# Optimization experiments

Hardware: AMD Instinct MI355X
Metric: run time of the kernel (lower is better)

## Reference

```python
import jax, jax.numpy as jnp
import numpy as np

PENALTY_FACTOR = 2.0
THRESHOLD = 0.01


def setup_inputs() -> dict:
    key = jax.random.key(0)
    k1, k2 = jax.random.split(key)
    B, N = 256, 65536
    prediction = jax.random.normal(k1, (B, N), dtype=jnp.float32)
    label = jax.random.normal(k2, (B, N), dtype=jnp.float32)
    return {"prediction": prediction, "label": label}


def _first_last_significant(mask, half):
    # mask: [B, half] bool. Returns per-row first/last True index,
    # defaulting to (0, half-1) when the row has no True entries
    # (matching the torch fallback branch).
    any_m = jnp.any(mask, axis=1)
    first = jnp.argmax(mask, axis=1)                      # 0 if all False
    last = (half - 1) - jnp.argmax(mask[:, ::-1], axis=1)  # half-1 if all False
    first = jnp.where(any_m, first, 0)
    last = jnp.where(any_m, last, half - 1)
    return first, last


def reference(prediction, label):
    B, N = label.shape
    half = N // 2
    label_real, label_imag = label[:, :half], label[:, half:]
    pred_real, pred_imag = prediction[:, :half], prediction[:, half:]

    label_phase = jnp.arctan2(label_imag, label_real)
    pred_phase = jnp.arctan2(pred_imag, pred_real)
    label_int = label_real ** 2 + label_imag ** 2
    pred_int = pred_real ** 2 + pred_imag ** 2

    fr, lr = _first_last_significant(jnp.abs(label_real) > THRESHOLD, half)
    fi, li = _first_last_significant(jnp.abs(label_imag) > THRESHOLD, half)

    idx = jnp.arange(half)[None, :]  # [1, half]
    w_real = jnp.where((idx < fr[:, None]) | (idx > lr[:, None]), PENALTY_FACTOR, 1.0)
    w_imag = jnp.where((idx < fi[:, None]) | (idx > li[:, None]), PENALTY_FACTOR, 1.0)

    mse_real = w_real * (pred_real - label_real) ** 2
    mse_imag = w_imag * (pred_imag - label_imag) ** 2
    mse_int = (pred_int - label_int) ** 2
    mse_phase = (pred_phase - label_phase) ** 2

    per_sample = (mse_real.mean(axis=1) + mse_imag.mean(axis=1)
                  + 50.0 * mse_int.mean(axis=1) + 0.0 * mse_phase.mean(axis=1))
    return per_sample.mean()
```

## Files before the change

### kernel.cpp

```cpp
#include <hip/hip_runtime.h>
#include <climits>

constexpr int HALF  = 32768;
constexpr int TPB   = 256;
constexpr int CHUNK = 2048;
constexpr int NCHNK = HALF / CHUNK;
constexpr float THRESH = 0.01f;

__global__ __launch_bounds__(TPB)
void main_kernel(const float* __restrict__ pred, const float* __restrict__ label,
                 float* __restrict__ part_sum, int4* __restrict__ part_idx)
{
    const int chunk = blockIdx.x, row = blockIdx.y;
    const int t = threadIdx.x, wave = t >> 6, lane = t & 63;

    const size_t rb4 = (size_t)row * (size_t)(2 * HALF / 4);
    const float4* lr4 = (const float4*)label + rb4;
    const float4* pr4 = (const float4*)pred + rb4;

    const int v0 = chunk * (CHUNK / 4) + t;
    const int v1 = v0 + TPB;
    const int H4 = HALF / 4;

    float4 a0 = lr4[v0],      a1 = lr4[v1];
    float4 b0 = lr4[v0 + H4], b1 = lr4[v1 + H4];
    float4 p0 = pr4[v0],      p1 = pr4[v1];
    float4 q0 = pr4[v0 + H4], q1 = pr4[v1 + H4];

    float sum = 0.f;
    int minr = INT_MAX, maxr = -1, mini = INT_MAX, maxi = -1;

#define STEP(ax, bx, px, qx, idx)                                 \
    {                                                             \
        float dr = (px) - (ax), di = (qx) - (bx);                 \
        float lint = (ax) * (ax) + (bx) * (bx);                   \
        float pint = (px) * (px) + (qx) * (qx);                   \
        float dd = pint - lint;                                   \
        sum += dr * dr + di * di + 50.f * dd * dd;                \
        if (fabsf(ax) > THRESH) {                                 \
            minr = min(minr, (idx)); maxr = max(maxr, (idx));     \
        }                                                         \
        if (fabsf(bx) > THRESH) {                                 \
            mini = min(mini, (idx)); maxi = max(maxi, (idx));     \
        }                                                         \
    }
    {
        const int base = v0 * 4;
        STEP(a0.x, b0.x, p0.x, q0.x, base + 0)
        STEP(a0.y, b0.y, p0.y, q0.y, base + 1)
        STEP(a0.z, b0.z, p0.z, q0.z, base + 2)
        STEP(a0.w, b0.w, p0.w, q0.w, base + 3)
    }
    {
        const int base = v1 * 4;
        STEP(a1.x, b1.x, p1.x, q1.x, base + 0)
        STEP(a1.y, b1.y, p1.y, q1.y, base + 1)
        STEP(a1.z, b1.z, p1.z, q1.z, base + 2)
        STEP(a1.w, b1.w, p1.w, q1.w, base + 3)
    }
#undef STEP

    #pragma unroll
    for (int off = 32; off > 0; off >>= 1) {
        sum += __shfl_down(sum, off);
        minr = min(minr, __shfl_down(minr, off));
        maxr = max(maxr, __shfl_down(maxr, off));
        mini = min(mini, __shfl_down(mini, off));
        maxi = max(maxi, __shfl_down(maxi, off));
    }

    __shared__ float s_sum[4];
    __shared__ int   s_idx[4][4];
    if (lane == 0) {
        s_sum[wave] = sum;
        s_idx[wave][0] = minr; s_idx[wave][1] = maxr;
        s_idx[wave][2] = mini; s_idx[wave][3] = maxi;
    }
    __syncthreads();
    if (t == 0) {
        float S = 0.f; int mr = INT_MAX, Mr = -1, mi = INT_MAX, Mi = -1;
        #pragma unroll
        for (int w = 0; w < 4; ++w) {
            S += s_sum[w];
            mr = min(mr, s_idx[w][0]); Mr = max(Mr, s_idx[w][1]);
            mi = min(mi, s_idx[w][2]); Mi = max(Mi, s_idx[w][3]);
        }
        const int slot = row * NCHNK + chunk;
        part_sum[slot] = S;
        part_idx[slot] = make_int4(mr, Mr, mi, Mi);
    }
}

__global__ __launch_bounds__(TPB)
void edge_kernel(const float* __restrict__ pred, const float* __restrict__ label,
                 const float* __restrict__ part_sum, const int4* __restrict__ part_idx,
                 float* __restrict__ row_tot)
{
    const int row = blockIdx.x;
    const int t = threadIdx.x, wave = t >> 6, lane = t & 63;

    float base = 0.f;
    int fr = INT_MAX, lastr = -1, fi = INT_MAX, lasti = -1;
    #pragma unroll
    for (int s = 0; s < NCHNK; ++s) {
        base += part_sum[row * NCHNK + s];
        int4 v = part_idx[row * NCHNK + s];
        fr = min(fr, v.x); lastr = max(lastr, v.y);
        fi = min(fi, v.z); lasti = max(lasti, v.w);
    }
    if (lastr < 0) { fr = 0; lastr = HALF - 1; }
    if (lasti < 0) { fi = 0; lasti = HALF - 1; }

    const float* Lr = label + (size_t)row * (2 * HALF);
    const float* Li = Lr + HALF;
    const float* Pr = pred + (size_t)row * (2 * HALF);
    const float* Pi = Pr + HALF;

    float ex = 0.f;
    for (int i = t; i < fr; i += TPB)               { float d = Pr[i] - Lr[i]; ex += d * d; }
    for (int i = lastr + 1 + t; i < HALF; i += TPB) { float d = Pr[i] - Lr[i]; ex += d * d; }
    for (int i = t; i < fi; i += TPB)               { float d = Pi[i] - Li[i]; ex += d * d; }
    for (int i = lasti + 1 + t; i < HALF; i += TPB) { float d = Pi[i] - Li[i]; ex += d * d; }

    #pragma unroll
    for (int off = 32; off > 0; off >>= 1) ex += __shfl_down(ex, off);
    __shared__ float s_ex[4];
    if (lane == 0) s_ex[wave] = ex;
    __syncthreads();
    if (t == 0)
        row_tot[row] = base + s_ex[0] + s_ex[1] + s_ex[2] + s_ex[3];
}

__global__ void finalize_kernel(const float* __restrict__ row_tot,
                                float* __restrict__ out, int rows)
{
    const int t = threadIdx.x;
    float v = 0.f;
    for (int i = t; i < rows; i += 256) v += row_tot[i];
    #pragma unroll
    for (int off = 32; off > 0; off >>= 1) v += __shfl_down(v, off);
    __shared__ float s[4];
    if ((t & 63) == 0) s[t >> 6] = v;
    __syncthreads();
    if (t == 0)
        out[0] = (s[0] + s[1] + s[2] + s[3]) * (1.0f / ((float)HALF * (float)rows));
}

extern "C" void kernel_launch(void* const* d_in, const int* in_sizes, int n_in,
                              void* d_out, int out_size, void* d_ws, size_t ws_size,
                              hipStream_t stream) {
    const float* pred  = (const float*)d_in[0];
    const float* label = (const float*)d_in[1];
    float* out = (float*)d_out;

    const int rows = in_sizes[0] / (2 * HALF);
    const int nslots = rows * NCHNK;

    float* part_sum = (float*)d_ws;
    int4*  part_idx = (int4*)((char*)d_ws + nslots * 4);
    float* row_tot  = (float*)((char*)d_ws + nslots * 4 + nslots * 16);

    dim3 gridA(NCHNK, rows);
    main_kernel<<<gridA, TPB, 0, stream>>>(pred, label, part_sum, part_idx);
    edge_kernel<<<rows, TPB, 0, stream>>>(pred, label, part_sum, part_idx, row_tot);
    finalize_kernel<<<1, 256, 0, stream>>>(row_tot, out, rows);
}
```

Measured before the change: 29.29 us.

## Fuse main, edge and finalize kernels into one cooperative kernel with grid syncs

Combines the three launches into a single cooperative kernel that uses grid-wide synchronization between the chunk reduction, per-row edge correction and final reduction phases. Intermediate partials are written and read with agent-scope atomic stores and loads. It is meant to remove inter-kernel launch gaps. The cooperative path is only used if occupancy allows all 4096 blocks to be co-resident, otherwise it falls back to the original three launches. Host-side occupancy queries are added on every call.

```diff
diff --git a/kernel.cpp b/kernel.cpp
--- a/kernel.cpp
+++ b/kernel.cpp
@@ -1,19 +1,36 @@
 #include <hip/hip_runtime.h>
+#include <hip/hip_cooperative_groups.h>
 #include <climits>
+
+namespace cg = cooperative_groups;
 
 constexpr int HALF  = 32768;
 constexpr int TPB   = 256;
 constexpr int CHUNK = 2048;
 constexpr int NCHNK = HALF / CHUNK;
+constexpr int ROWS  = 256;
+constexpr int NBLK  = NCHNK * ROWS;
 constexpr float THRESH = 0.01f;
 
-__global__ __launch_bounds__(TPB)
-void main_kernel(const float* __restrict__ pred, const float* __restrict__ label,
-                 float* __restrict__ part_sum, int4* __restrict__ part_idx)
-{
-    const int chunk = blockIdx.x, row = blockIdx.y;
-    const int t = threadIdx.x, wave = t >> 6, lane = t & 63;
-
+__device__ __forceinline__ void st_ag(float* p, float v) {
+    __hip_atomic_store(p, v, __ATOMIC_RELAXED, __HIP_MEMORY_SCOPE_AGENT);
+}
+__device__ __forceinline__ float ld_ag(const float* p) {
+    return __hip_atomic_load(p, __ATOMIC_RELAXED, __HIP_MEMORY_SCOPE_AGENT);
+}
+__device__ __forceinline__ void st_ag_i(int* p, int v) {
+    __hip_atomic_store(p, v, __ATOMIC_RELAXED, __HIP_MEMORY_SCOPE_AGENT);
+}
+__device__ __forceinline__ int ld_ag_i(const int* p) {
+    return __hip_atomic_load(p, __ATOMIC_RELAXED, __HIP_MEMORY_SCOPE_AGENT);
+}
+
+template <typename SUMF, typename IDXF>
+__device__ __forceinline__ void phase1_body(const float* __restrict__ pred,
+                                            const float* __restrict__ label,
+                                            int chunk, int row, int t, int wave, int lane,
+                                            SUMF&& emit_sum, IDXF&& emit_idx)
+{
     const size_t rb4 = (size_t)row * (size_t)(2 * HALF / 4);
     const float4* lr4 = (const float4*)label + rb4;
     const float4* pr4 = (const float4*)pred + rb4;
@@ -85,31 +102,136 @@
             mr = min(mr, s_idx[w][0]); Mr = max(Mr, s_idx[w][1]);
             mi = min(mi, s_idx[w][2]); Mi = max(Mi, s_idx[w][3]);
         }
+        emit_sum(S);
+        emit_idx(mr, Mr, mi, Mi);
+    }
+}
+
+__global__ __launch_bounds__(TPB, 8)
+void fused_kernel(const float* __restrict__ pred, const float* __restrict__ label,
+                  float* __restrict__ part_sum, int* __restrict__ part_idx,
+                  float* __restrict__ row_tot, float* __restrict__ out)
+{
+    cg::grid_group grid = cg::this_grid();
+    const int bid = blockIdx.x;
+    const int chunk = bid & (NCHNK - 1);
+    const int row = bid >> 4;
+    const int t = threadIdx.x, wave = t >> 6, lane = t & 63;
+
+    {
         const int slot = row * NCHNK + chunk;
-        part_sum[slot] = S;
-        part_idx[slot] = make_int4(mr, Mr, mi, Mi);
-    }
+        phase1_body(pred, label, chunk, row, t, wave, lane,
+            [&](float S) { st_ag(&part_sum[slot], S); },
+            [&](int mr, int Mr, int mi, int Mi) {
+                st_ag_i(&part_idx[slot * 4 + 0], mr);
+                st_ag_i(&part_idx[slot * 4 + 1], Mr);
+                st_ag_i(&part_idx[slot * 4 + 2], mi);
+                st_ag_i(&part_idx[slot * 4 + 3], Mi);
+            });
+    }
+
+    grid.sync();
+
+    if (bid < ROWS) {
+        const int r = bid;
+        __shared__ float sh_sum[NCHNK];
+        __shared__ int   sh_i[NCHNK][4];
+        if (t < NCHNK) {
+            const int slot = r * NCHNK + t;
+            sh_sum[t]  = ld_ag(&part_sum[slot]);
+            sh_i[t][0] = ld_ag_i(&part_idx[slot * 4 + 0]);
+            sh_i[t][1] = ld_ag_i(&part_idx[slot * 4 + 1]);
+            sh_i[t][2] = ld_ag_i(&part_idx[slot * 4 + 2]);
+            sh_i[t][3] = ld_ag_i(&part_idx[slot * 4 + 3]);
+        }
+        __syncthreads();
+
+        __shared__ float sh_base;
+        __shared__ int   sh_b[4];
+        if (t == 0) {
+            float S = 0.f; int fr = INT_MAX, lr = -1, fi = INT_MAX, li = -1;
+            #pragma unroll
+            for (int c = 0; c < NCHNK; ++c) {
+                S += sh_sum[c];
+                fr = min(fr, sh_i[c][0]); lr = max(lr, sh_i[c][1]);
+                fi = min(fi, sh_i[c][2]); li = max(li, sh_i[c][3]);
+            }
+            if (lr < 0) { fr = 0; lr = HALF - 1; }
+            if (li < 0) { fi = 0; li = HALF - 1; }
+            sh_base = S;
+            sh_b[0] = fr; sh_b[1] = lr; sh_b[2] = fi; sh_b[3] = li;
+        }
+        __syncthreads();
+        const int fr = sh_b[0], lr = sh_b[1], fi = sh_b[2], li = sh_b[3];
+
+        const float* Lr = label + (size_t)r * (2 * HALF);
+        const float* Li = Lr + HALF;
+        const float* Pr = pred + (size_t)r * (2 * HALF);
+        const float* Pi = Pr + HALF;
+
+        float ex = 0.f;
+        for (int i = t; i < fr; i += TPB)            { float d = Pr[i] - Lr[i]; ex += d * d; }
+        for (int i = lr + 1 + t; i < HALF; i += TPB) { float d = Pr[i] - Lr[i]; ex += d * d; }
+        for (int i = t; i < fi; i += TPB)            { float d = Pi[i] - Li[i]; ex += d * d; }
+        for (int i = li + 1 + t; i < HALF; i += TPB) { float d = Pi[i] - Li[i]; ex += d * d; }
+
+        #pragma unroll
+        for (int off = 32; off > 0; off >>= 1) ex += __shfl_down(ex, off);
+        __shared__ float s_ex[4];
+        if (lane == 0) s_ex[wave] = ex;
+        __syncthreads();
+        if (t == 0)
+            st_ag(&row_tot[r], sh_base + s_ex[0] + s_ex[1] + s_ex[2] + s_ex[3]);
+    }
+
+    grid.sync();
+
+    if (bid == 0) {
+        float v = (t < ROWS) ? ld_ag(&row_tot[t]) : 0.f;
+        #pragma unroll
+        for (int off = 32; off > 0; off >>= 1) v += __shfl_down(v, off);
+        __shared__ float sf[4];
+        if (lane == 0) sf[wave] = v;
+        __syncthreads();
+        if (t == 0)
+            out[0] = (sf[0] + sf[1] + sf[2] + sf[3]) * (1.0f / ((float)HALF * (float)ROWS));
+    }
+}
+
+__global__ __launch_bounds__(TPB)
+void main_kernel(const float* __restrict__ pred, const float* __restrict__ label,
+                 float* __restrict__ part_sum, int* __restrict__ part_idx)
+{
+    const int chunk = blockIdx.x, row = blockIdx.y;
+    const int t = threadIdx.x, wave = t >> 6, lane = t & 63;
+    const int slot = row * NCHNK + chunk;
+    phase1_body(pred, label, chunk, row, t, wave, lane,
+        [&](float S) { part_sum[slot] = S; },
+        [&](int mr, int Mr, int mi, int Mi) {
+            part_idx[slot * 4 + 0] = mr; part_idx[slot * 4 + 1] = Mr;
+            part_idx[slot * 4 + 2] = mi; part_idx[slot * 4 + 3] = Mi;
+        });
 }
 
 __global__ __launch_bounds__(TPB)
 void edge_kernel(const float* __restrict__ pred, const float* __restrict__ label,
-                 const float* __restrict__ part_sum, const int4* __restrict__ part_idx,
+                 const float* __restrict__ part_sum, const int* __restrict__ part_idx,
                  float* __restrict__ row_tot)
 {
     const int row = blockIdx.x;
     const int t = threadIdx.x, wave = t >> 6, lane = t & 63;
 
     float base = 0.f;
-    int fr = INT_MAX, lastr = -1, fi = INT_MAX, lasti = -1;
+    int fr = INT_MAX, lr = -1, fi = INT_MAX, li = -1;
     #pragma unroll
     for (int s = 0; s < NCHNK; ++s) {
-        base += part_sum[row * NCHNK + s];
-        int4 v = part_idx[row * NCHNK + s];
-        fr = min(fr, v.x); lastr = max(lastr, v.y);
-        fi = min(fi, v.z); lasti = max(lasti, v.w);
-    }
-    if (lastr < 0) { fr = 0; lastr = HALF - 1; }
-    if (lasti < 0) { fi = 0; lasti = HALF - 1; }
+        const int slot = row * NCHNK + s;
+        base += part_sum[slot];
+        fr = min(fr, part_idx[slot * 4 + 0]); lr = max(lr, part_idx[slot * 4 + 1]);
+        fi = min(fi, part_idx[slot * 4 + 2]); li = max(li, part_idx[slot * 4 + 3]);
+    }
+    if (lr < 0) { fr = 0; lr = HALF - 1; }
+    if (li < 0) { fi = 0; li = HALF - 1; }
 
     const float* Lr = label + (size_t)row * (2 * HALF);
     const float* Li = Lr + HALF;
@@ -117,10 +239,10 @@
     const float* Pi = Pr + HALF;
 
     float ex = 0.f;
-    for (int i = t; i < fr; i += TPB)               { float d = Pr[i] - Lr[i]; ex += d * d; }
-    for (int i = lastr + 1 + t; i < HALF; i += TPB) { float d = Pr[i] - Lr[i]; ex += d * d; }
-    for (int i = t; i < fi; i += TPB)               { float d = Pi[i] - Li[i]; ex += d * d; }
-    for (int i = lasti + 1 + t; i < HALF; i += TPB) { float d = Pi[i] - Li[i]; ex += d * d; }
+    for (int i = t; i < fr; i += TPB)            { float d = Pr[i] - Lr[i]; ex += d * d; }
+    for (int i = lr + 1 + t; i < HALF; i += TPB) { float d = Pr[i] - Lr[i]; ex += d * d; }
+    for (int i = t; i < fi; i += TPB)            { float d = Pi[i] - Li[i]; ex += d * d; }
+    for (int i = li + 1 + t; i < HALF; i += TPB) { float d = Pi[i] - Li[i]; ex += d * d; }
 
     #pragma unroll
     for (int off = 32; off > 0; off >>= 1) ex += __shfl_down(ex, off);
@@ -153,15 +275,30 @@
     const float* label = (const float*)d_in[1];
     float* out = (float*)d_out;
 
-    const int rows = in_sizes[0] / (2 * HALF);
-    const int nslots = rows * NCHNK;
-
+    const int nslots = ROWS * NCHNK;
     float* part_sum = (float*)d_ws;
-    int4*  part_idx = (int4*)((char*)d_ws + nslots * 4);
+    int*   part_idx = (int*)((char*)d_ws + nslots * 4);
     float* row_tot  = (float*)((char*)d_ws + nslots * 4 + nslots * 16);
 
-    dim3 gridA(NCHNK, rows);
+    int dev = 0; hipGetDevice(&dev);
+    int num_cu = 0;
+    hipDeviceGetAttribute(&num_cu, hipDeviceAttributeMultiprocessorCount, dev);
+    int max_blk_per_cu = 0;
+    hipError_t occ_err = hipOccupancyMaxActiveBlocksPerMultiprocessor(
+        &max_blk_per_cu, fused_kernel, TPB, 0);
+
+    bool coop_ok = (occ_err == hipSuccess) && (max_blk_per_cu * num_cu >= NBLK);
+
+    if (coop_ok) {
+        void* args[] = { (void*)&pred, (void*)&label, (void*)&part_sum,
+                         (void*)&part_idx, (void*)&row_tot, (void*)&out };
+        hipError_t err = hipLaunchCooperativeKernel(
+            (const void*)fused_kernel, dim3(NBLK), dim3(TPB), args, 0, stream);
+        if (err == hipSuccess) return;
+    }
+
+    dim3 gridA(NCHNK, ROWS);
     main_kernel<<<gridA, TPB, 0, stream>>>(pred, label, part_sum, part_idx);
-    edge_kernel<<<rows, TPB, 0, stream>>>(pred, label, part_sum, part_idx, row_tot);
-    finalize_kernel<<<1, 256, 0, stream>>>(row_tot, out, rows);
-}
+    edge_kernel<<<ROWS, TPB, 0, stream>>>(pred, label, part_sum, part_idx, row_tot);
+    finalize_kernel<<<1, TPB, 0, stream>>>(row_tot, out, ROWS);
+}
```

Result: no change. 29.65 us (+1.2%).
